# Performance work log

Measured on AMD Instinct MI355X. Metric: run time of the kernel, lower is better.

## Reference

```python
import jax, jax.numpy as jnp
import numpy as np

# ---- Butterworth lowpass design, identical math to scipy.signal.butter(4, 0.5, 'low') ----
ORDER = 4
WN = 4000.0 / (0.5 * 16000.0)  # = 0.5 (normalized cutoff, Nyquist = 1)
_fs2 = 4.0                      # 2 * fs with fs = 2 (scipy bilinear convention)
_warped = _fs2 * np.tan(np.pi * WN / 4.0)
# analog Butterworth prototype poles, scaled to warped cutoff
_k = np.arange(1, ORDER + 1)
_p = _warped * np.exp(1j * np.pi * (2 * _k + ORDER - 1) / (2 * ORDER))
_gain = _warped ** ORDER
# bilinear transform: poles -> digital, zeros all at z = -1
_pd = (_fs2 + _p) / (_fs2 - _p)
_kd = _gain / np.real(np.prod(_fs2 - _p))
B_COEF = np.real(_kd * np.poly(-np.ones(ORDER))).astype(np.float32)  # [b0..b4]
A_COEF = np.real(np.poly(_pd)).astype(np.float32)                   # [1, a1..a4]


def _lfilter(x):
    """Direct-form II transposed IIR, matching scipy.signal.lfilter(b, a, x).
    x: [B, T] -> y: [B, T]. State z: [B, order]."""
    b = jnp.asarray(B_COEF)
    a = jnp.asarray(A_COEF)
    bsz = x.shape[0]
    z0 = jnp.zeros((bsz, ORDER), x.dtype)

    def step(z, xt):  # z: [B, 4], xt: [B]
        y = b[0] * xt + z[:, 0]
        z_shift = jnp.concatenate([z[:, 1:], jnp.zeros((bsz, 1), z.dtype)], axis=1)
        z_new = z_shift + b[1:] * xt[:, None] - a[1:] * y[:, None]
        return z_new, y

    _, ys = jax.lax.scan(step, z0, x.T)  # scan over time: ys [T, B]
    return ys.T


def setup_inputs() -> dict:
    key = jax.random.key(0)
    x = jax.random.normal(key, (256, 65536, 1), dtype=jnp.float32)
    return {"x": x}


def reference(x):
    # Training-time layer filters with prob%; the reference implements the
    # deterministic filter branch (the expensive path being kernelized).
    y = _lfilter(x[:, :, 0])
    return y[:, :, None]
```

## Files before the change

kernel.cpp:

```cpp
#include <hip/hip_runtime.h>
#include <cmath>
#include <complex>

#ifndef M_PI
#define M_PI 3.14159265358979323846
#endif

namespace {

constexpr int NT     = 256;
constexpr int CHUNK  = 32;
constexpr int WARM   = 32;
constexpr int REGION = NT * CHUNK;
constexpr int T_LEN  = 65536;

struct Coefs { float b0, b1, b2, b3, b4, a1, a2, a3, a4; };

__device__ __forceinline__ int lds_addr4(int o, int tg) {
    return (o << 5) + ((tg ^ (o & 7)) << 2);
}

__global__ __launch_bounds__(NT, 5) void butter_kernel(
        const float* __restrict__ x, float* __restrict__ y, Coefs c) {
    __shared__ float lds[REGION];

    const int tid = threadIdx.x;
    const int bpr = T_LEN / REGION;
    const int row = blockIdx.x / bpr;
    const int bir = blockIdx.x % bpr;
    const size_t base = (size_t)row * T_LEN + (size_t)bir * REGION;
    const float4* __restrict__ xin = (const float4*)(x + base);

    float4 sv[8];
#pragma unroll
    for (int k = 0; k < 8; ++k) sv[k] = xin[k * NT + tid];

    float4 wv[WARM / 4];
    if (tid == 0) {
#pragma unroll
        for (int i = 0; i < WARM / 4; ++i) wv[i] = make_float4(0.f, 0.f, 0.f, 0.f);
        if (bir != 0) {
            const float4* __restrict__ xw = (const float4*)(x + base - WARM);
#pragma unroll
            for (int i = 0; i < WARM / 4; ++i) wv[i] = xw[i];
        }
    }
#pragma unroll
    for (int k = 0; k < 8; ++k) {
        int i4 = k * NT + tid;
        *(float4*)&lds[lds_addr4(i4 >> 3, i4 & 7)] = sv[k];
    }
    __syncthreads();

    if (tid != 0) {
#pragma unroll
        for (int tg = 0; tg < WARM / 4; ++tg)
            wv[tg] = *(const float4*)&lds[lds_addr4(tid - 1, tg)];
    }
    __syncthreads();

    float z0 = 0.f, z1 = 0.f, z2 = 0.f, z3 = 0.f;

#define STEP_Y(xv, yv)                                   \
    do {                                                 \
        yv = fmaf(c.b0, (xv), z0);                       \
        z0 = fmaf(-c.a1, (yv), fmaf(c.b1, (xv), z1));    \
        z1 = fmaf(-c.a2, (yv), fmaf(c.b2, (xv), z2));    \
        z2 = fmaf(-c.a3, (yv), fmaf(c.b3, (xv), z3));    \
        z3 = fmaf(-c.a4, (yv), c.b4 * (xv));             \
    } while (0)

#pragma unroll
    for (int i = 0; i < WARM / 4; ++i) {
        float yd;
        STEP_Y(wv[i].x, yd); STEP_Y(wv[i].y, yd);
        STEP_Y(wv[i].z, yd); STEP_Y(wv[i].w, yd);
        (void)yd;
    }

#pragma unroll
    for (int tg = 0; tg < CHUNK / 4; ++tg) {
        int a = lds_addr4(tid, tg);
        float4 xv = *(const float4*)&lds[a];
        float4 yv;
        STEP_Y(xv.x, yv.x); STEP_Y(xv.y, yv.y);
        STEP_Y(xv.z, yv.z); STEP_Y(xv.w, yv.w);
        *(float4*)&lds[a] = yv;
    }
#undef STEP_Y
    __syncthreads();

    float4* __restrict__ yout = (float4*)(y + base);
#pragma unroll
    for (int k = 0; k < 8; ++k) {
        int i4 = k * NT + tid;
        yout[i4] = *(const float4*)&lds[lds_addr4(i4 >> 3, i4 & 7)];
    }
}

Coefs make_coefs() {
    const int ORDER = 4;
    const double wn  = 4000.0 / (0.5 * 16000.0);
    const double fs2 = 4.0;
    const double warped = fs2 * std::tan(M_PI * wn / 4.0);
    std::complex<double> pd[4];
    std::complex<double> prod(1.0, 0.0);
    for (int k = 1; k <= ORDER; ++k) {
        double ang = M_PI * (2.0 * k + ORDER - 1.0) / (2.0 * ORDER);
        std::complex<double> p = warped * std::exp(std::complex<double>(0.0, ang));
        prod *= (fs2 - p);
        pd[k - 1] = (fs2 + p) / (fs2 - p);
    }
    double kd = std::pow(warped, ORDER) / prod.real();
    double b[5] = { kd, 4.0 * kd, 6.0 * kd, 4.0 * kd, kd };
    std::complex<double> a[5] = { {1,0}, {0,0}, {0,0}, {0,0}, {0,0} };
    for (int k = 0; k < ORDER; ++k)
        for (int j = k + 1; j >= 1; --j) a[j] -= pd[k] * a[j - 1];
    Coefs c;
    c.b0 = (float)b[0]; c.b1 = (float)b[1]; c.b2 = (float)b[2];
    c.b3 = (float)b[3]; c.b4 = (float)b[4];
    c.a1 = (float)a[1].real(); c.a2 = (float)a[2].real();
    c.a3 = (float)a[3].real(); c.a4 = (float)a[4].real();
    return c;
}

}

extern "C" void kernel_launch(void* const* d_in, const int* in_sizes, int n_in,
                              void* d_out, int out_size, void* d_ws, size_t ws_size,
                              hipStream_t stream) {
    (void)in_sizes; (void)n_in; (void)d_ws; (void)ws_size;
    const float* x = (const float*)d_in[0];
    float* y = (float*)d_out;
    Coefs c = make_coefs();
    const int nblocks = out_size / REGION;
    butter_kernel<<<nblocks, NT, 0, stream>>>(x, y, c);
}
```

Baseline: 111.5 us.

## Make each wavefront self-contained to drop block-wide barriers

```diff
diff --git a/kernel.cpp b/kernel.cpp
--- a/kernel.cpp
+++ b/kernel.cpp
@@ -35,16 +35,19 @@
 #pragma unroll
     for (int k = 0; k < 8; ++k) sv[k] = xin[k * NT + tid];
 
+    const bool lane0 = ((tid & 63) == 0);
     float4 wv[WARM / 4];
-    if (tid == 0) {
+    if (lane0) {
 #pragma unroll
         for (int i = 0; i < WARM / 4; ++i) wv[i] = make_float4(0.f, 0.f, 0.f, 0.f);
-        if (bir != 0) {
-            const float4* __restrict__ xw = (const float4*)(x + base - WARM);
+        if (!(bir == 0 && tid == 0)) {
+            const float4* __restrict__ xw =
+                (const float4*)(x + base + (size_t)tid * CHUNK - WARM);
 #pragma unroll
             for (int i = 0; i < WARM / 4; ++i) wv[i] = xw[i];
         }
     }
+
 #pragma unroll
     for (int k = 0; k < 8; ++k) {
         int i4 = k * NT + tid;
@@ -52,12 +55,15 @@
     }
     __syncthreads();
 
-    if (tid != 0) {
+    if (!lane0) {
 #pragma unroll
         for (int tg = 0; tg < WARM / 4; ++tg)
             wv[tg] = *(const float4*)&lds[lds_addr4(tid - 1, tg)];
     }
-    __syncthreads();
+    float4 mv[CHUNK / 4];
+#pragma unroll
+    for (int tg = 0; tg < CHUNK / 4; ++tg)
+        mv[tg] = *(const float4*)&lds[lds_addr4(tid, tg)];
 
     float z0 = 0.f, z1 = 0.f, z2 = 0.f, z3 = 0.f;
 
@@ -80,20 +86,21 @@
 
 #pragma unroll
     for (int tg = 0; tg < CHUNK / 4; ++tg) {
-        int a = lds_addr4(tid, tg);
-        float4 xv = *(const float4*)&lds[a];
         float4 yv;
-        STEP_Y(xv.x, yv.x); STEP_Y(xv.y, yv.y);
-        STEP_Y(xv.z, yv.z); STEP_Y(xv.w, yv.w);
-        *(float4*)&lds[a] = yv;
+        STEP_Y(mv[tg].x, yv.x); STEP_Y(mv[tg].y, yv.y);
+        STEP_Y(mv[tg].z, yv.z); STEP_Y(mv[tg].w, yv.w);
+        *(float4*)&lds[lds_addr4(tid, tg)] = yv;
     }
 #undef STEP_Y
-    __syncthreads();
 
+    asm volatile("" ::: "memory");
+    __builtin_amdgcn_wave_barrier();
+
+    const int w = tid >> 6, l = tid & 63;
     float4* __restrict__ yout = (float4*)(y + base);
 #pragma unroll
-    for (int k = 0; k < 8; ++k) {
-        int i4 = k * NT + tid;
+    for (int j = 0; j < 8; ++j) {
+        int i4 = (w << 9) + (j << 6) + l;
         yout[i4] = *(const float4*)&lds[lds_addr4(i4 >> 3, i4 & 7)];
     }
 }
```

Result: no change. 110.4 us (-1.1%).
